# Kernel optimization log

Hardware: AMD Instinct MI355X
Metric: run time of the kernel (lower is better)

Reference implementation:

```python
import jax, jax.numpy as jnp
import numpy as np
import math

EMB = 768
HEADS = 12
HEAD_DIM = EMB // HEADS
FF = 3072
EPS = 1e-5


def setup_inputs() -> dict:
    key = jax.random.key(0)
    ks = jax.random.split(key, 12)
    s = 0.02
    return {
        "x": jax.random.normal(ks[0], (8, 1024, EMB), dtype=jnp.float32),
        "qkv_w": jax.random.normal(ks[1], (EMB, 3 * EMB), dtype=jnp.float32) * s,
        "qkv_b": jnp.zeros((3 * EMB,), dtype=jnp.float32),
        "out_w": jax.random.normal(ks[2], (EMB, EMB), dtype=jnp.float32) * s,
        "out_b": jnp.zeros((EMB,), dtype=jnp.float32),
        "ln1_g": jnp.ones((EMB,), dtype=jnp.float32),
        "ln1_b": jnp.zeros((EMB,), dtype=jnp.float32),
        "ln2_g": jnp.ones((EMB,), dtype=jnp.float32),
        "ln2_b": jnp.zeros((EMB,), dtype=jnp.float32),
        "fc1_w": jax.random.normal(ks[3], (EMB, FF), dtype=jnp.float32) * s,
        "fc1_b": jnp.zeros((FF,), dtype=jnp.float32),
        "fc2_w": jax.random.normal(ks[4], (FF, EMB), dtype=jnp.float32) * s,
        "fc2_b": jnp.zeros((EMB,), dtype=jnp.float32),
    }


def layernorm(x, g, b):
    mu = jnp.mean(x, axis=-1, keepdims=True)
    var = jnp.var(x, axis=-1, keepdims=True)
    return (x - mu) * jax.lax.rsqrt(var + EPS) * g + b


def new_gelu(x):
    c = math.sqrt(2.0 / math.pi)
    return 0.5 * x * (1.0 + jnp.tanh(c * (x + 0.044715 * x * x * x)))


def reference(x, qkv_w, qkv_b, out_w, out_b, ln1_g, ln1_b, ln2_g, ln2_b,
              fc1_w, fc1_b, fc2_w, fc2_b):
    B, S, _ = x.shape
    # --- attention sublayer (pre-LN) ---
    h = layernorm(x, ln1_g, ln1_b)
    qkv = h @ qkv_w + qkv_b                      # [B,S,3E]
    q, k, v = jnp.split(qkv, 3, axis=-1)
    def heads(t):
        return t.reshape(B, S, HEADS, HEAD_DIM).transpose(0, 2, 1, 3)  # [B,H,S,D]
    q, k, v = heads(q), heads(k), heads(v)
    scores = jnp.einsum('bhsd,bhtd->bhst', q, k) / math.sqrt(HEAD_DIM)
    probs = jax.nn.softmax(scores, axis=-1)
    attn = jnp.einsum('bhst,bhtd->bhsd', probs, v)
    attn = attn.transpose(0, 2, 1, 3).reshape(B, S, EMB)
    attn = attn @ out_w + out_b
    x = x + attn
    # --- MLP sublayer (pre-LN) ---
    h = layernorm(x, ln2_g, ln2_b)
    h = new_gelu(h @ fc1_w + fc1_b)
    h = h @ fc2_w + fc2_b
    return x + h
```

## Files before the change

kernel.cpp:

```cpp
#include <hip/hip_runtime.h>

typedef __bf16 bf16x8 __attribute__((ext_vector_type(8)));
typedef __bf16 bf16x4 __attribute__((ext_vector_type(4)));
typedef __bf16 bf16x2 __attribute__((ext_vector_type(2)));
typedef float  f32x4  __attribute__((ext_vector_type(4)));
typedef float  f32x16 __attribute__((ext_vector_type(16)));
typedef unsigned int uintx4 __attribute__((ext_vector_type(4)));

#define EMB 768
#define HEADS 12
#define HD 64
#define FF 3072
#define SEQ 1024
#define BATCH 8
#define ROWS (BATCH*SEQ)
#define QKVSZ ((size_t)BATCH*HEADS*SEQ*HD)
#define LOG2E 1.44269504088896f

__device__ __forceinline__ void gload16(const void* g, void* l) {
    __builtin_amdgcn_global_load_lds(
        (const __attribute__((address_space(1))) unsigned int*)g,
        (__attribute__((address_space(3))) unsigned int*)l,
        16, 0, 0);
}

__device__ __forceinline__ unsigned int pkbf16(float lo, float hi) {
    bf16x2 w = { (__bf16)lo, (__bf16)hi };
    return __builtin_bit_cast(unsigned int, w);
}

__global__ __launch_bounds__(256) void ln_kernel(const float* __restrict__ x,
        const float* __restrict__ g, const float* __restrict__ b,
        __bf16* __restrict__ out)
{
    int row = blockIdx.x;
    int tid = threadIdx.x;
    const float* xr = x + (size_t)row * EMB;
    float v0 = xr[tid], v1 = xr[tid + 256], v2 = xr[tid + 512];
    float s  = v0 + v1 + v2;
    float ss = v0*v0 + v1*v1 + v2*v2;
    #pragma unroll
    for (int off = 32; off >= 1; off >>= 1) {
        s  += __shfl_xor(s, off);
        ss += __shfl_xor(ss, off);
    }
    __shared__ float red[2][4];
    int wave = tid >> 6;
    if ((tid & 63) == 0) { red[0][wave] = s; red[1][wave] = ss; }
    __syncthreads();
    s  = red[0][0] + red[0][1] + red[0][2] + red[0][3];
    ss = red[1][0] + red[1][1] + red[1][2] + red[1][3];
    float mu  = s * (1.0f / EMB);
    float var = ss * (1.0f / EMB) - mu * mu;
    float inv = rsqrtf(var + 1e-5f);
    __bf16* orow = out + (size_t)row * EMB;
    orow[tid]       = (__bf16)((v0 - mu) * inv * g[tid]       + b[tid]);
    orow[tid + 256] = (__bf16)((v1 - mu) * inv * g[tid + 256] + b[tid + 256]);
    orow[tid + 512] = (__bf16)((v2 - mu) * inv * g[tid + 512] + b[tid + 512]);
}

__global__ __launch_bounds__(256) void transpose_convert(const float* __restrict__ W,
        __bf16* __restrict__ WT, int K, int N)
{
    __shared__ float t[32][33];
    int nb = blockIdx.x * 32, kb = blockIdx.y * 32;
    int tx = threadIdx.x, ty = threadIdx.y;
    #pragma unroll
    for (int i = 0; i < 32; i += 8)
        t[ty + i][tx] = W[(size_t)(kb + ty + i) * N + nb + tx];
    __syncthreads();
    #pragma unroll
    for (int i = 0; i < 32; i += 8)
        WT[(size_t)(nb + ty + i) * K + kb + tx] = (__bf16)t[tx][ty + i];
}

__global__ __launch_bounds__(256) void vtrans_kernel(const __bf16* __restrict__ V,
        __bf16* __restrict__ Vt)
{
    __shared__ __bf16 t[64][72];
    int bh = blockIdx.x >> 4, st = blockIdx.x & 15;
    const __bf16* Vp = V + ((size_t)bh * SEQ + st * 64) * HD;
    int r  = threadIdx.x >> 3;
    int c0 = (threadIdx.x & 7) * 8;
    #pragma unroll
    for (int rep = 0; rep < 2; rep++)
        *(bf16x8*)&t[r + rep*32][c0] = *(const bf16x8*)(Vp + (size_t)(r + rep*32) * HD + c0);
    __syncthreads();
    #pragma unroll
    for (int rep = 0; rep < 2; rep++) {
        int dd = r + rep*32;
        bf16x8 o;
        #pragma unroll
        for (int j = 0; j < 8; j++) o[j] = t[c0 + j][dd];
        *(bf16x8*)(Vt + ((size_t)bh * HD + dd) * SEQ + st * 64 + c0) = o;
    }
}

template<int EPI>
__global__ __launch_bounds__(256) void gemm_bt(
    const __bf16* __restrict__ A, const __bf16* __restrict__ BT,
    const float* __restrict__ bias, const float* __restrict__ resid,
    void* __restrict__ outp, int M, int N, int K)
{
    __shared__ __bf16 Al[128][32];
    __shared__ __bf16 Bl[128][32];
    int tid  = threadIdx.x;
    int lane = tid & 63, wave = tid >> 6;
    int wr = wave >> 1, wc = wave & 1;
    int lr = lane & 15, lg = lane >> 4;
    int bn = blockIdx.x * 128, bm = blockIdx.y * 128;

    int srow = wave * 16 + (lane >> 2);
    int scol = (lane & 3) * 8;
    const __bf16* Ag0 = A  + (size_t)(bm + srow) * K + scol;
    const __bf16* Ag1 = Ag0 + (size_t)64 * K;
    const __bf16* Bg0 = BT + (size_t)(bn + srow) * K + scol;
    const __bf16* Bg1 = Bg0 + (size_t)64 * K;
    __bf16* lA0 = &Al[wave * 16][0];
    __bf16* lA1 = &Al[64 + wave * 16][0];
    __bf16* lB0 = &Bl[wave * 16][0];
    __bf16* lB1 = &Bl[64 + wave * 16][0];

    f32x4 acc[4][4];
    #pragma unroll
    for (int i = 0; i < 4; i++)
        #pragma unroll
        for (int j = 0; j < 4; j++) acc[i][j] = (f32x4){0.f, 0.f, 0.f, 0.f};

    for (int k0 = 0; k0 < K; k0 += 32) {
        gload16(Ag0 + k0, lA0);
        gload16(Ag1 + k0, lA1);
        gload16(Bg0 + k0, lB0);
        gload16(Bg1 + k0, lB1);
        __syncthreads();
        bf16x8 af[4], bfr[4];
        #pragma unroll
        for (int mi = 0; mi < 4; mi++) af[mi]  = *(const bf16x8*)&Al[wr*64 + mi*16 + lr][lg*8];
        #pragma unroll
        for (int ni = 0; ni < 4; ni++) bfr[ni] = *(const bf16x8*)&Bl[wc*64 + ni*16 + lr][lg*8];
        #pragma unroll
        for (int mi = 0; mi < 4; mi++)
            #pragma unroll
            for (int ni = 0; ni < 4; ni++)
                acc[mi][ni] = __builtin_amdgcn_mfma_f32_16x16x32_bf16(af[mi], bfr[ni], acc[mi][ni], 0, 0, 0);
        __syncthreads();
    }

    #pragma unroll
    for (int mi = 0; mi < 4; mi++) {
        int row = bm + wr*64 + mi*16 + lg*4;
        #pragma unroll
        for (int ni = 0; ni < 4; ni++) {
            int col = bn + wc*64 + ni*16 + lr;
            float bv = bias[col];
            #pragma unroll
            for (int j = 0; j < 4; j++) {
                int r = row + j;
                float v = acc[mi][ni][j] + bv;
                if (EPI == 0) {
                    int which = col / 768;
                    int cc = col - which * 768;
                    int hh = cc >> 6, dd = cc & 63;
                    int bb = r >> 10, s = r & 1023;
                    if (which == 0) v *= 0.125f * LOG2E;
                    ((__bf16*)outp)[(size_t)which * QKVSZ +
                        ((((size_t)bb * HEADS + hh) << 10) + s) * HD + dd] = (__bf16)v;
                } else if (EPI == 1) {
                    ((float*)outp)[(size_t)r * N + col] = v + resid[(size_t)r * N + col];
                } else {
                    float u = 0.7978845608028654f * (v + 0.044715f * v * v * v);
                    float e = __expf(2.0f * u);
                    float th = 1.0f - 2.0f / (e + 1.0f);
                    ((__bf16*)outp)[(size_t)r * N + col] = (__bf16)(0.5f * v * (1.0f + th));
                }
            }
        }
    }
}

__device__ __forceinline__ void loadK(bf16x8 (&dst)[8], const __bf16* Kp, int t, int lq, int hi) {
    #pragma unroll
    for (int kb = 0; kb < 2; kb++)
        #pragma unroll
        for (int dc = 0; dc < 4; dc++)
            dst[kb*4+dc] = *(const bf16x8*)(Kp + (size_t)(t*64 + kb*32 + lq) * HD + dc*16 + hi*8);
}

__global__ __launch_bounds__(256) void attn_kernel(
    const __bf16* __restrict__ Q, const __bf16* __restrict__ Km,
    const __bf16* __restrict__ Vt, __bf16* __restrict__ Aout)
{
    int xcd  = blockIdx.x & 7;
    int idx  = blockIdx.x >> 3;
    int bh   = xcd * 12 + (idx % 12);
    int qblk = idx / 12;
    int bb = bh / HEADS, hh = bh % HEADS;
    const __bf16* Qp = Q  + (size_t)bh * SEQ * HD;
    const __bf16* Kp = Km + (size_t)bh * SEQ * HD;
    const __bf16* Vp = Vt + (size_t)bh * HD * SEQ;
    int lane = threadIdx.x & 63, wave = threadIdx.x >> 6;
    int lq = lane & 31, hi = lane >> 5;
    int q0 = qblk * 128 + wave * 32;

    bf16x8 qf[4];
    #pragma unroll
    for (int dc = 0; dc < 4; dc++)
        qf[dc] = *(const bf16x8*)(Qp + (size_t)(q0 + lq) * HD + dc*16 + hi*8);

    f32x16 o0, o1;
    #pragma unroll
    for (int i = 0; i < 16; i++) { o0[i] = 0.f; o1[i] = 0.f; }
    float m = -1e30f, l = 0.0f;

    bf16x8 kfA[8], kfB[8];
    loadK(kfA, Kp, 0, lq, hi);

#define ATTN_TILE(KF, KFN, T)                                                        \
    do {                                                                             \
        bf16x8 vf[8];                                                                \
        _Pragma("unroll")                                                            \
        for (int nb = 0; nb < 2; nb++)                                               \
            _Pragma("unroll")                                                        \
            for (int ks = 0; ks < 4; ks++)                                           \
                vf[nb*4+ks] = *(const bf16x8*)(Vp + (size_t)(nb*32 + lq) * SEQ       \
                                               + (T)*64 + ks*16 + hi*8);             \
        f32x16 st0, st1;                                                             \
        _Pragma("unroll")                                                            \
        for (int i = 0; i < 16; i++) { st0[i] = 0.f; st1[i] = 0.f; }                 \
        _Pragma("unroll")                                                            \
        for (int dc = 0; dc < 4; dc++)                                               \
            st0 = __builtin_amdgcn_mfma_f32_32x32x16_bf16(KF[dc], qf[dc], st0, 0, 0, 0); \
        _Pragma("unroll")                                                            \
        for (int dc = 0; dc < 4; dc++)                                               \
            st1 = __builtin_amdgcn_mfma_f32_32x32x16_bf16(KF[4+dc], qf[dc], st1, 0, 0, 0); \
        loadK(KFN, Kp, (T)+1, lq, hi);                                               \
        float pmax = st0[0];                                                         \
        _Pragma("unroll")                                                            \
        for (int i = 1; i < 16; i++) pmax = fmaxf(pmax, st0[i]);                     \
        _Pragma("unroll")                                                            \
        for (int i = 0; i < 16; i++) pmax = fmaxf(pmax, st1[i]);                     \
        pmax = fmaxf(pmax, __shfl_xor(pmax, 32));                                    \
        if (__any(pmax > m + 11.5f)) {                                               \
            float mn = fmaxf(m, pmax);                                               \
            float sc = exp2f(m - mn);                                                \
            _Pragma("unroll")                                                        \
            for (int r = 0; r < 16; r++) {                                           \
                float scr = __shfl(sc, (r & 3) + 8*(r >> 2) + 4*hi);                 \
                o0[r] *= scr; o1[r] *= scr;                                          \
            }                                                                        \
            l *= sc; m = mn;                                                         \
        }                                                                            \
        float p[32];                                                                 \
        _Pragma("unroll")                                                            \
        for (int i = 0; i < 16; i++) { p[i] = exp2f(st0[i] - m);                     \
                                       p[16+i] = exp2f(st1[i] - m); }                \
        float ps = 0.f;                                                              \
        _Pragma("unroll")                                                            \
        for (int i = 0; i < 32; i++) ps += p[i];                                     \
        ps += __shfl_xor(ps, 32);                                                    \
        l += ps;                                                                     \
        _Pragma("unroll")                                                            \
        for (int ks = 0; ks < 4; ks++) {                                             \
            unsigned int pa_ = pkbf16(p[ks*8+0], p[ks*8+1]);                         \
            unsigned int pc_ = pkbf16(p[ks*8+2], p[ks*8+3]);                         \
            unsigned int pb_ = pkbf16(p[ks*8+4], p[ks*8+5]);                         \
            unsigned int pd_ = pkbf16(p[ks*8+6], p[ks*8+7]);                         \
            asm("v_permlane32_swap_b32 %0, %1" : "+v"(pb_), "+v"(pa_));              \
            asm("v_permlane32_swap_b32 %0, %1" : "+v"(pd_), "+v"(pc_));              \
            uintx4 w_ = { pa_, pc_, pb_, pd_ };                                      \
            bf16x8 paf = __builtin_bit_cast(bf16x8, w_);                             \
            o0 = __builtin_amdgcn_mfma_f32_32x32x16_bf16(paf, vf[ks],   o0, 0, 0, 0); \
            o1 = __builtin_amdgcn_mfma_f32_32x32x16_bf16(paf, vf[4+ks], o1, 0, 0, 0); \
        }                                                                            \
    } while (0)

    #pragma unroll 1
    for (int t = 0; t < 16; t += 2) {
        ATTN_TILE(kfA, kfB, t);
        ATTN_TILE(kfB, kfA, t + 1);
    }
#undef ATTN_TILE

    float linv = 1.0f / l;
    #pragma unroll
    for (int r = 0; r < 16; r++) {
        int crow = (r & 3) + 8*(r >> 2) + 4*hi;
        float sc = __shfl(linv, crow);
        int q = q0 + crow;
        __bf16* dst = Aout + ((size_t)bb * SEQ + q) * EMB + hh * HD + lq;
        dst[0]  = (__bf16)(o0[r] * sc);
        dst[32] = (__bf16)(o1[r] * sc);
    }
}

extern "C" void kernel_launch(void* const* d_in, const int* in_sizes, int n_in,
                              void* d_out, int out_size, void* d_ws, size_t ws_size,
                              hipStream_t stream) {
    const float* x      = (const float*)d_in[0];
    const float* qkv_w  = (const float*)d_in[1];
    const float* qkv_b  = (const float*)d_in[2];
    const float* out_w  = (const float*)d_in[3];
    const float* out_b  = (const float*)d_in[4];
    const float* ln1_g  = (const float*)d_in[5];
    const float* ln1_b  = (const float*)d_in[6];
    const float* ln2_g  = (const float*)d_in[7];
    const float* ln2_b  = (const float*)d_in[8];
    const float* fc1_w  = (const float*)d_in[9];
    const float* fc1_b  = (const float*)d_in[10];
    const float* fc2_w  = (const float*)d_in[11];
    const float* fc2_b  = (const float*)d_in[12];

    char* ws = (char*)d_ws;
    __bf16* wqkvT  = (__bf16*)(ws + 0);
    __bf16* woutT  = (__bf16*)(ws + 3538944);
    __bf16* wfc1T  = (__bf16*)(ws + 4718592);
    __bf16* wfc2T  = (__bf16*)(ws + 9437184);
    float*  x1     = (float*) (ws + 14155776);
    __bf16* vt     = (__bf16*)(ws + 14155776);
    __bf16* hbuf   = (__bf16*)(ws + 39321600);
    __bf16* qbuf   = (__bf16*)(ws + 51904512);
    __bf16* attn   = (__bf16*)(ws + 89653248);
    __bf16* fc1out = (__bf16*)(ws + 51904512);

    transpose_convert<<<dim3(2304/32, 768/32),  dim3(32,8), 0, stream>>>(qkv_w, wqkvT, 768, 2304);
    transpose_convert<<<dim3(768/32,  768/32),  dim3(32,8), 0, stream>>>(out_w, woutT, 768, 768);
    transpose_convert<<<dim3(3072/32, 768/32),  dim3(32,8), 0, stream>>>(fc1_w, wfc1T, 768, 3072);
    transpose_convert<<<dim3(768/32,  3072/32), dim3(32,8), 0, stream>>>(fc2_w, wfc2T, 3072, 768);

    ln_kernel<<<ROWS, 256, 0, stream>>>(x, ln1_g, ln1_b, hbuf);
    gemm_bt<0><<<dim3(2304/128, ROWS/128), 256, 0, stream>>>(hbuf, wqkvT, qkv_b, nullptr, qbuf, ROWS, 2304, 768);
    vtrans_kernel<<<BATCH*HEADS*(SEQ/64), 256, 0, stream>>>(qbuf + 2*QKVSZ, vt);
    attn_kernel<<<BATCH*HEADS*(SEQ/128), 256, 0, stream>>>(qbuf, qbuf + QKVSZ, vt, attn);
    gemm_bt<1><<<dim3(768/128, ROWS/128), 256, 0, stream>>>(attn, woutT, out_b, x, x1, ROWS, 768, 768);
    ln_kernel<<<ROWS, 256, 0, stream>>>(x1, ln2_g, ln2_b, hbuf);
    gemm_bt<2><<<dim3(3072/128, ROWS/128), 256, 0, stream>>>(hbuf, wfc1T, fc1_b, nullptr, fc1out, ROWS, 3072, 768);
    gemm_bt<1><<<dim3(768/128, ROWS/128), 256, 0, stream>>>(fc1out, wfc2T, fc2_b, x1, (float*)d_out, ROWS, 768, 3072);
}
```

Baseline: 450.7 us.

## Replace GEMM with triple-buffered 256x128 pipelined kernel using swizzled LDS

Replaces the single-buffered 128x128x32 GEMM with a 512-thread kernel that computes 256x128 tiles with K-step 64. Tiles are loaded straight into LDS with a three-stage async global_load_lds pipeline, using XOR-swizzled layout to avoid bank conflicts, plus a block-index swizzle for L2 locality and setprio around the MFMA bursts. The aim is to hide global memory latency and cut barrier overhead in the GEMMs that dominate runtime. It needs 144 KB of dynamic LDS, which allows one block per CU, and it relies on hand-placed waitcnt counts that must match the number of loads issued per stage.

```diff
diff --git a/kernel.cpp b/kernel.cpp
--- a/kernel.cpp
+++ b/kernel.cpp
@@ -97,29 +97,46 @@
 }
 
 template<int EPI>
-__global__ __launch_bounds__(256) void gemm_bt(
+__global__ __launch_bounds__(512) void gemm_pipe(
     const __bf16* __restrict__ A, const __bf16* __restrict__ BT,
     const float* __restrict__ bias, const float* __restrict__ resid,
     void* __restrict__ outp, int M, int N, int K)
 {
-    __shared__ __bf16 Al[128][32];
-    __shared__ __bf16 Bl[128][32];
-    int tid  = threadIdx.x;
-    int lane = tid & 63, wave = tid >> 6;
-    int wr = wave >> 1, wc = wave & 1;
-    int lr = lane & 15, lg = lane >> 4;
-    int bn = blockIdx.x * 128, bm = blockIdx.y * 128;
-
-    int srow = wave * 16 + (lane >> 2);
-    int scol = (lane & 3) * 8;
-    const __bf16* Ag0 = A  + (size_t)(bm + srow) * K + scol;
-    const __bf16* Ag1 = Ag0 + (size_t)64 * K;
-    const __bf16* Bg0 = BT + (size_t)(bn + srow) * K + scol;
-    const __bf16* Bg1 = Bg0 + (size_t)64 * K;
-    __bf16* lA0 = &Al[wave * 16][0];
-    __bf16* lA1 = &Al[64 + wave * 16][0];
-    __bf16* lB0 = &Bl[wave * 16][0];
-    __bf16* lB1 = &Bl[64 + wave * 16][0];
+    extern __shared__ char lds[];
+    const int tid = threadIdx.x;
+    const int lane = tid & 63, wid = tid >> 6;
+    const int wr = wid >> 1, wc = wid & 1;
+    const int lr = lane & 15, lg = lane >> 4;
+
+    int nbx = gridDim.x;
+    int nwg = nbx * gridDim.y;
+    int orig = blockIdx.y * nbx + blockIdx.x;
+    int q8 = nwg >> 3;
+    int swz = (orig & 7) * q8 + (orig >> 3);
+    int bm = (swz / nbx) * 256;
+    int bn = (swz % nbx) * 128;
+
+    const int srow = tid >> 3;
+    const int scolb = ((tid & 7) * 16) ^ ((srow & 7) << 4);
+    const char* Ag = (const char*)A  + ((size_t)(bm + srow) * K) * 2 + scolb;
+    const char* Bg = (const char*)BT + ((size_t)(bn + srow) * K) * 2 + scolb;
+    const size_t rstride = (size_t)64 * K * 2;
+
+#define STAGE_P(t)                                                          \
+    do {                                                                    \
+        char* base_ = lds + ((t) % 3) * 49152;                              \
+        size_t kb_ = (size_t)(t) * 128;                                     \
+        _Pragma("unroll")                                                   \
+        for (int i_ = 0; i_ < 4; i_++)                                      \
+            gload16(Ag + i_ * rstride + kb_, base_ + i_ * 8192 + tid * 16); \
+        _Pragma("unroll")                                                   \
+        for (int i_ = 0; i_ < 2; i_++)                                      \
+            gload16(Bg + i_ * rstride + kb_, base_ + 32768 + i_ * 8192 + tid * 16); \
+    } while (0)
+
+    const int kxor = (lr & 7) << 4;
+    const int abase = (wr * 64 + lr) * 128;
+    const int bbase = 32768 + (wc * 64 + lr) * 128;
 
     f32x4 acc[4][4];
     #pragma unroll
@@ -127,31 +144,52 @@
         #pragma unroll
         for (int j = 0; j < 4; j++) acc[i][j] = (f32x4){0.f, 0.f, 0.f, 0.f};
 
-    for (int k0 = 0; k0 < K; k0 += 32) {
-        gload16(Ag0 + k0, lA0);
-        gload16(Ag1 + k0, lA1);
-        gload16(Bg0 + k0, lB0);
-        gload16(Bg1 + k0, lB1);
-        __syncthreads();
-        bf16x8 af[4], bfr[4];
-        #pragma unroll
-        for (int mi = 0; mi < 4; mi++) af[mi]  = *(const bf16x8*)&Al[wr*64 + mi*16 + lr][lg*8];
-        #pragma unroll
-        for (int ni = 0; ni < 4; ni++) bfr[ni] = *(const bf16x8*)&Bl[wc*64 + ni*16 + lr][lg*8];
-        #pragma unroll
-        for (int mi = 0; mi < 4; mi++)
+    const int NT = K >> 6;
+    STAGE_P(0);
+    STAGE_P(1);
+    asm volatile("s_waitcnt vmcnt(6)" ::: "memory");
+    __builtin_amdgcn_s_barrier();
+    __builtin_amdgcn_sched_barrier(0);
+
+    for (int t = 0; t < NT; ++t) {
+        if (t + 2 < NT) STAGE_P(t + 2);
+        const char* base = lds + (t % 3) * 49152;
+        #pragma unroll
+        for (int ksub = 0; ksub < 2; ++ksub) {
+            const int ko = ((ksub ? 64 : 0) + lg * 16) ^ kxor;
+            bf16x8 af[4], bfr[4];
+            #pragma unroll
+            for (int mi = 0; mi < 4; mi++)
+                af[mi] = *(const bf16x8*)(base + abase + mi * 2048 + ko);
             #pragma unroll
             for (int ni = 0; ni < 4; ni++)
-                acc[mi][ni] = __builtin_amdgcn_mfma_f32_16x16x32_bf16(af[mi], bfr[ni], acc[mi][ni], 0, 0, 0);
-        __syncthreads();
-    }
+                bfr[ni] = *(const bf16x8*)(base + bbase + ni * 2048 + ko);
+            __builtin_amdgcn_s_setprio(1);
+            #pragma unroll
+            for (int mi = 0; mi < 4; mi++)
+                #pragma unroll
+                for (int ni = 0; ni < 4; ni++)
+                    acc[mi][ni] = __builtin_amdgcn_mfma_f32_16x16x32_bf16(af[mi], bfr[ni], acc[mi][ni], 0, 0, 0);
+            __builtin_amdgcn_s_setprio(0);
+        }
+        asm volatile("s_waitcnt lgkmcnt(0)" ::: "memory");
+        __builtin_amdgcn_sched_barrier(0);
+        if (t + 2 < NT) {
+            asm volatile("s_waitcnt vmcnt(6)" ::: "memory");
+        } else if (t + 1 < NT) {
+            asm volatile("s_waitcnt vmcnt(0)" ::: "memory");
+        }
+        __builtin_amdgcn_s_barrier();
+        __builtin_amdgcn_sched_barrier(0);
+    }
+#undef STAGE_P
 
     #pragma unroll
     for (int mi = 0; mi < 4; mi++) {
-        int row = bm + wr*64 + mi*16 + lg*4;
+        int row = bm + wr * 64 + mi * 16 + lg * 4;
         #pragma unroll
         for (int ni = 0; ni < 4; ni++) {
-            int col = bn + wc*64 + ni*16 + lr;
+            int col = bn + wc * 64 + ni * 16 + lr;
             float bv = bias[col];
             #pragma unroll
             for (int j = 0; j < 4; j++) {
@@ -322,17 +360,21 @@
     __bf16* attn   = (__bf16*)(ws + 89653248);
     __bf16* fc1out = (__bf16*)(ws + 51904512);
 
+    hipFuncSetAttribute((const void*)gemm_pipe<0>, hipFuncAttributeMaxDynamicSharedMemorySize, 147456);
+    hipFuncSetAttribute((const void*)gemm_pipe<1>, hipFuncAttributeMaxDynamicSharedMemorySize, 147456);
+    hipFuncSetAttribute((const void*)gemm_pipe<2>, hipFuncAttributeMaxDynamicSharedMemorySize, 147456);
+
     transpose_convert<<<dim3(2304/32, 768/32),  dim3(32,8), 0, stream>>>(qkv_w, wqkvT, 768, 2304);
     transpose_convert<<<dim3(768/32,  768/32),  dim3(32,8), 0, stream>>>(out_w, woutT, 768, 768);
     transpose_convert<<<dim3(3072/32, 768/32),  dim3(32,8), 0, stream>>>(fc1_w, wfc1T, 768, 3072);
     transpose_convert<<<dim3(768/32,  3072/32), dim3(32,8), 0, stream>>>(fc2_w, wfc2T, 3072, 768);
 
     ln_kernel<<<ROWS, 256, 0, stream>>>(x, ln1_g, ln1_b, hbuf);
-    gemm_bt<0><<<dim3(2304/128, ROWS/128), 256, 0, stream>>>(hbuf, wqkvT, qkv_b, nullptr, qbuf, ROWS, 2304, 768);
+    gemm_pipe<0><<<dim3(2304/128, ROWS/256), 512, 147456, stream>>>(hbuf, wqkvT, qkv_b, nullptr, qbuf, ROWS, 2304, 768);
     vtrans_kernel<<<BATCH*HEADS*(SEQ/64), 256, 0, stream>>>(qbuf + 2*QKVSZ, vt);
     attn_kernel<<<BATCH*HEADS*(SEQ/128), 256, 0, stream>>>(qbuf, qbuf + QKVSZ, vt, attn);
-    gemm_bt<1><<<dim3(768/128, ROWS/128), 256, 0, stream>>>(attn, woutT, out_b, x, x1, ROWS, 768, 768);
+    gemm_pipe<1><<<dim3(768/128, ROWS/256), 512, 147456, stream>>>(attn, woutT, out_b, x, x1, ROWS, 768, 768);
     ln_kernel<<<ROWS, 256, 0, stream>>>(x1, ln2_g, ln2_b, hbuf);
-    gemm_bt<2><<<dim3(3072/128, ROWS/128), 256, 0, stream>>>(hbuf, wfc1T, fc1_b, nullptr, fc1out, ROWS, 3072, 768);
-    gemm_bt<1><<<dim3(768/128, ROWS/128), 256, 0, stream>>>(fc1out, wfc2T, fc2_b, x1, (float*)d_out, ROWS, 768, 3072);
-}
+    gemm_pipe<2><<<dim3(3072/128, ROWS/256), 512, 147456, stream>>>(hbuf, wfc1T, fc1_b, nullptr, fc1out, ROWS, 3072, 768);
+    gemm_pipe<1><<<dim3(768/128, ROWS/256), 512, 147456, stream>>>(fc1out, wfc2T, fc2_b, x1, (float*)d_out, ROWS, 768, 3072);
+}
```

Result: faster. 409.4 us (-9.2%).
